# Kernel tuning notes

Measured on AMD Instinct MI355X. Metric: run time of the kernel, lower is better.

## Reference

```python
import jax, jax.numpy as jnp
import numpy as np

N_QUBITS = 12
N_LAYERS = 4
BATCH = 4096
OUT_DIM = 12


def _ry(theta):
    theta = jnp.asarray(theta, jnp.float32)
    c, s = jnp.cos(theta / 2), jnp.sin(theta / 2)
    U = jnp.stack([jnp.stack([c, -s], -1), jnp.stack([s, c], -1)], -2)
    return U.astype(jnp.complex64)


def _rx(theta):
    theta = jnp.asarray(theta, jnp.float32)
    c = jnp.cos(theta / 2).astype(jnp.complex64)
    s = (-1j) * jnp.sin(theta / 2).astype(jnp.complex64)
    return jnp.stack([jnp.stack([c, s], -1), jnp.stack([s, c], -1)], -2)


def _rz(theta):
    theta = jnp.asarray(theta, jnp.float32)
    e = jnp.exp((-0.5j) * theta.astype(jnp.complex64))
    z = jnp.zeros_like(e)
    return jnp.stack([jnp.stack([e, z], -1), jnp.stack([z, jnp.conj(e)], -1)], -2)


def _apply_1q(psi, U, w):
    # psi: (B,) + (2,)*n; U: (2,2) shared gate or (B,2,2) per-sample gate
    psi = jnp.moveaxis(psi, w + 1, 1)
    if U.ndim == 2:
        psi = jnp.einsum('ij,bj...->bi...', U, psi)
    else:
        psi = jnp.einsum('bij,bj...->bi...', U, psi)
    return jnp.moveaxis(psi, 1, w + 1)


def _cnot(psi, c, t):
    # flip target axis where control bit == 1
    psi = jnp.moveaxis(psi, (c + 1, t + 1), (1, 2))
    psi = psi.at[:, 1].set(psi[:, 1, ::-1])
    return jnp.moveaxis(psi, (1, 2), (c + 1, t + 1))


def _pauli_z_signs(n):
    idx = np.arange(2 ** n)
    bits = (idx[None, :] >> (n - 1 - np.arange(n))[:, None]) & 1  # wire 0 = MSB
    return jnp.asarray(1.0 - 2.0 * bits, jnp.float32)  # (n, 2^n)


def _quantum_forward(x, quantum_weights):
    b, n = x.shape[0], N_QUBITS
    # tf.nn.l2_normalize(sample, axis=0) per sample
    xn = x * jax.lax.rsqrt(jnp.maximum(jnp.sum(x * x, axis=1, keepdims=True), 1e-12))
    # angle encoding: pi * x / (max|x| + 1e-8)
    angles = jnp.pi * xn / (jnp.max(jnp.abs(xn), axis=1, keepdims=True) + 1e-8)
    psi = jnp.zeros((b, 2 ** n), jnp.complex64).at[:, 0].set(1.0)
    psi = psi.reshape((b,) + (2,) * n)
    # data encoding: RY(angles[i]) on wire i (per-sample batched gates)
    for i in range(n):
        psi = _apply_1q(psi, _ry(angles[:, i]), i)
    # variational layers: RX/RY/RZ per qubit, then CNOT ring
    for layer in range(N_LAYERS):
        base = layer * 3 * n
        for i in range(n):
            p = base + 3 * i
            psi = _apply_1q(psi, _rx(quantum_weights[p]), i)
            psi = _apply_1q(psi, _ry(quantum_weights[p + 1]), i)
            psi = _apply_1q(psi, _rz(quantum_weights[p + 2]), i)
        for i in range(n):
            psi = _cnot(psi, i, (i + 1) % n)
    psi = psi.reshape(b, -1)
    probs = jnp.real(psi) ** 2 + jnp.imag(psi) ** 2  # (B, 2^n)
    return probs @ _pauli_z_signs(n).T  # (B, n): <Z_i> per qubit


def setup_inputs() -> dict:
    key = jax.random.key(0)
    k1, k2, k3 = jax.random.split(key, 3)
    n_params = 3 * N_QUBITS * N_LAYERS
    return {
        'x': jax.random.normal(k1, (BATCH, N_QUBITS), jnp.float32),
        'quantum_weights': jax.random.uniform(k2, (n_params,), jnp.float32, -0.05, 0.05),
        'dense_w': jax.random.normal(k3, (N_QUBITS, OUT_DIM), jnp.float32) / np.sqrt(N_QUBITS),
        'dense_b': jnp.zeros((OUT_DIM,), jnp.float32),
    }


def reference(x, quantum_weights, dense_w, dense_b):
    q = _quantum_forward(x, quantum_weights)
    return jnp.tanh(q @ dense_w + dense_b)
```

## Files before the change

### kernel.cpp

```cpp
#include <hip/hip_runtime.h>
#include <math.h>

#define NQ   12
#define NL   4
#define GBLK 256
#define QBLK 512
#define SOFF(i) ((i) * 8192)

typedef float v4f  __attribute__((ext_vector_type(4)));
typedef __fp16 v8h __attribute__((ext_vector_type(8)));

__device__ __forceinline__ constexpr int sigma_inv_c(int i) {
    int j = i;
    for (int c = 0; c < NQ; ++c) {
        int t = (c + 1) % NQ;
        int cb = (j >> (NQ - 1 - c)) & 1;
        j ^= cb << (NQ - 1 - t);
    }
    return j;
}

__device__ __forceinline__ constexpr int lswz(int l) {
    return l ^ (((l >> 3) ^ (l >> 7)) & 7);
}

__device__ __forceinline__ unsigned pk2(float a, float b) {
    return __builtin_bit_cast(unsigned, __builtin_amdgcn_cvt_pkrtz(a, b));
}

__device__ __forceinline__ int fslot(int k, int n) {
    return ((k >> 3) * 16 + n) * 8 + (k & 7);
}

__global__ __launch_bounds__(GBLK) void gate_kernel(
    const float* __restrict__ qw, __fp16* __restrict__ gout)
{
    __shared__ float G[NQ][8];
    const int t = threadIdx.x;
    const int mat = blockIdx.x;
    const int layer = mat / 3, ph = mat - 3 * layer;
    if (t < NQ) {
        const int p = layer * 3 * NQ + 3 * t;
        float t1 = qw[p], t2 = qw[p + 1], t3 = qw[p + 2];
        float a, b, c, d, gr, h;
        sincosf(0.5f * t1, &b, &a);
        sincosf(0.5f * t2, &d, &c);
        sincosf(0.5f * t3, &h, &gr);
        float m00r =  c * a, m00i =  d * b;
        float m01r = -d * a, m01i = -c * b;
        float m10r =  d * a, m10i = -c * b;
        float m11r =  c * a, m11i = -d * b;
        float* g = G[t];
        g[0] = gr * m00r + h * m00i;  g[1] = gr * m00i - h * m00r;
        g[2] = gr * m01r + h * m01i;  g[3] = gr * m01i - h * m01r;
        g[4] = gr * m10r - h * m10i;  g[5] = gr * m10i + h * m10r;
        g[6] = gr * m11r - h * m11i;  g[7] = gr * m11i + h * m11r;
    }
    __syncthreads();
    const int n = t & 15, r = t >> 4;
    const int wbase = (ph == 0) ? 8 : (ph == 1) ? 4 : 0;
    float cr = 1.f, ci = 0.f;
    #pragma unroll
    for (int b = 0; b < 4; ++b) {
        const float* g = G[wbase + b];
        const int rb = (r >> (3 - b)) & 1, nb = (n >> (3 - b)) & 1;
        const float er = g[(nb * 2 + rb) * 2], ei = g[(nb * 2 + rb) * 2 + 1];
        const float xr = cr * er - ci * ei, xi = cr * ei + ci * er;
        cr = xr; ci = xi;
    }
    __fp16* b1 = gout + (mat * 2 + 0) * 512;
    __fp16* b2 = gout + (mat * 2 + 1) * 512;
    b1[fslot(2 * r, n)]     = (__fp16)cr;
    b1[fslot(2 * r + 1, n)] = (__fp16)(-ci);
    b2[fslot(2 * r, n)]     = (__fp16)ci;
    b2[fslot(2 * r + 1, n)] = (__fp16)cr;
}

#define READ_FRAGS(AF, SRC)                                                 \
    _Pragma("unroll")                                                       \
    for (int j = 0; j < 2; ++j)                                             \
        AF[j] = __builtin_bit_cast(v8h, *(const uint4*)&sh[(SRC) +          \
                    lswz((((wv) << 6) | ((2 * qh + j) << 4) | nn) * 4 + g) * 8]);

#define BLOAD(MAT)                                                          \
    const v8h b1 = gf[((MAT) * 2 + 0) * 64 + lane];                         \
    const v8h b2 = gf[((MAT) * 2 + 1) * 64 + lane];

#define MFMA_ONE(AF)                                                        \
    _Pragma("unroll")                                                       \
    for (int j = 0; j < 2; ++j) {                                           \
        d1[j] = __builtin_amdgcn_mfma_f32_16x16x32_f16(AF[j], b1, zf, 0, 0, 0); \
        d2[j] = __builtin_amdgcn_mfma_f32_16x16x32_f16(AF[j], b2, zf, 0, 0, 0); \
    }

#define SCHB __builtin_amdgcn_sched_barrier(0);

#define WRITE_COLS(DST)                                                     \
    _Pragma("unroll")                                                       \
    for (int j = 0; j < 2; ++j) {                                           \
        const int CCn = (nn << 4) | (wv << 2) | (2 * qh + j);               \
        *(uint4*)&sh[(DST) + lswz(CCn * 4 + g) * 8] =                       \
            make_uint4(pk2(d1[j].x, d2[j].x), pk2(d1[j].y, d2[j].y),        \
                       pk2(d1[j].z, d2[j].z), pk2(d1[j].w, d2[j].w));       \
    }

#define WRITE_SIGMA(DST)                                                    \
    _Pragma("unroll")                                                       \
    for (int j = 0; j < 2; ++j) {                                           \
        const int iq = ifix ^ (j ? sq1 : sq0);                              \
        _Pragma("unroll")                                                   \
        for (int rg = 0; rg < 4; ++rg) {                                    \
            const int ii = iq ^ sigma_inv_c(rg);                            \
            *(unsigned*)&sh[(DST) + lswz(ii >> 2) * 8 + (ii & 3) * 2] =     \
                pk2(d1[j][rg], d2[j][rg]);                                  \
        }                                                                   \
    }

#define WHT_EPI(OFF)                                                        \
    { float p8[8];                                                          \
      _Pragma("unroll")                                                     \
      for (int j = 0; j < 2; ++j)                                           \
          _Pragma("unroll")                                                 \
          for (int rg = 0; rg < 4; ++rg)                                    \
              p8[j * 4 + rg] = d1[j][rg] * d1[j][rg] + d2[j][rg] * d2[j][rg]; \
      _Pragma("unroll")                                                     \
      for (int st = 1; st < 8; st <<= 1) {                                  \
          _Pragma("unroll")                                                 \
          for (int i = 0; i < 8; ++i) {                                     \
              if (!(i & st)) {                                              \
                  const float a = p8[i], b = p8[i ^ st];                    \
                  p8[i] = a + b; p8[i ^ st] = a - b;                        \
              }                                                             \
          }                                                                 \
      }                                                                     \
      float vals[NQ];                                                       \
      _Pragma("unroll")                                                     \
      for (int w = 0; w < NQ; ++w) {                                        \
          const int sb = 11 - w;                                            \
          const int f3 = (sigma_inv_c(0x20) >> sb) & 1;                     \
          const int f2 = (sigma_inv_c(0x10) >> sb) & 1;                     \
          const int f1 = (sigma_inv_c(2)    >> sb) & 1;                     \
          const int f0 = (sigma_inv_c(1)    >> sb) & 1;                     \
          const float v = p8[f2 * 4 + f1 * 2 + f0];                         \
          const int sgn = ((ifix >> sb) & 1) ^ (f3 & qh);                   \
          vals[w] = sgn ? -v : v;                                           \
      }                                                                     \
      _Pragma("unroll")                                                     \
      for (int m = 1; m <= 8; m <<= 1) {                                    \
          _Pragma("unroll")                                                 \
          for (int w = 0; w < NQ; ++w) vals[w] += __shfl_xor(vals[w], m);   \
      }                                                                     \
      if ((lane & 15) == 0) {                                               \
          _Pragma("unroll")                                                 \
          for (int w = 0; w < NQ; ++w)                                      \
              red[(OFF) + W * 48 + (lane >> 4) * 12 + w] = vals[w];         \
      } }

__global__ __launch_bounds__(QBLK) void qsim_kernel(
    const float* __restrict__ x,
    const __fp16* __restrict__ gates,
    const float* __restrict__ dw,
    const float* __restrict__ db,
    float* __restrict__ out,
    int batch)
{
    __shared__ __align__(16) __fp16 sh[32768];
    float* xv    = (float*)sh;
    float* enc_c = (float*)sh + 64;
    float* enc_s = (float*)sh + 128;
    float* red   = (float*)sh;

    const int tid  = threadIdx.x;
    const int lane = tid & 63;
    const int W    = tid >> 6;
    const int wv   = W & 3;
    const int qh   = W >> 2;
    const int base = 4 * blockIdx.x;
    int ss[4];
    #pragma unroll
    for (int i = 0; i < 4; ++i) {
        int s = base + i;
        ss[i] = (s < batch) ? s : batch - 1;
    }
    const int nn = lane & 15, g = lane >> 4;
    const v8h* gf = (const v8h*)gates;
    const v4f zf = {0.f, 0.f, 0.f, 0.f};

    if (tid < 4 * NQ) {
        const int smp = tid / NQ, j = tid - smp * NQ;
        xv[tid] = x[ss[smp] * NQ + j];
    }
    __syncthreads();
    if (tid < 4 * NQ) {
        const int b0 = (tid / NQ) * NQ;
        float sum = 0.f;
        #pragma unroll
        for (int j = 0; j < NQ; ++j) sum += xv[b0 + j] * xv[b0 + j];
        float inv = rsqrtf(fmaxf(sum, 1e-12f));
        float mx = 0.f;
        #pragma unroll
        for (int j = 0; j < NQ; ++j) mx = fmaxf(mx, fabsf(xv[b0 + j] * inv));
        float ang = 3.14159265358979323846f * (xv[tid] * inv) / (mx + 1e-8f);
        float cc, sn;
        sincosf(0.5f * ang, &sn, &cc);
        enc_c[tid] = cc; enc_s[tid] = sn;
    }
    __syncthreads();

    v8h af0[2], af1[2], af2[2], af3[2];
    #define PICK(SMP, WW, B) ((B) ? enc_s[(SMP) * NQ + (WW)] : enc_c[(SMP) * NQ + (WW)])
    #define INIT_AF(AF, SMP)                                                \
    {   float R4[4];                                                        \
        _Pragma("unroll")                                                   \
        for (int t = 0; t < 4; ++t) {                                       \
            const int r = 4 * g + t;                                        \
            R4[t] = PICK(SMP, 8, (r >> 3) & 1) * PICK(SMP, 9, (r >> 2) & 1) \
                  * PICK(SMP, 10, (r >> 1) & 1) * PICK(SMP, 11, r & 1);     \
        }                                                                   \
        const float Pfix = PICK(SMP, 0, (wv >> 1) & 1) * PICK(SMP, 1, wv & 1) \
                         * PICK(SMP, 4, (nn >> 3) & 1) * PICK(SMP, 5, (nn >> 2) & 1) \
                         * PICK(SMP, 6, (nn >> 1) & 1) * PICK(SMP, 7, nn & 1); \
        _Pragma("unroll")                                                   \
        for (int j = 0; j < 2; ++j) {                                       \
            const float Pq = Pfix * PICK(SMP, 2, qh) * PICK(SMP, 3, j);     \
            _Pragma("unroll")                                               \
            for (int t = 0; t < 4; ++t) {                                   \
                AF[j][2 * t]     = (__fp16)(Pq * R4[t]);                    \
                AF[j][2 * t + 1] = (__fp16)0.f;                             \
            }                                                               \
        }                                                                   \
    }
    INIT_AF(af0, 0)
    INIT_AF(af1, 1)
    INIT_AF(af2, 2)
    INIT_AF(af3, 3)
    #undef PICK
    __syncthreads();

    const int ifix = sigma_inv_c((nn << 8) | (wv << 6) | (g << 2));
    const int sq0 = qh ? sigma_inv_c(0x20) : 0;
    const int sq1 = qh ? sigma_inv_c(0x30) : sigma_inv_c(0x10);

    v4f d1[2], d2[2];
    #define READ4                                                           \
        READ_FRAGS(af0, SOFF(0)) READ_FRAGS(af1, SOFF(1))                   \
        READ_FRAGS(af2, SOFF(2)) READ_FRAGS(af3, SOFF(3))
    #define COLS4(MAT)                                                      \
        { BLOAD(MAT)                                                        \
          MFMA_ONE(af0) WRITE_COLS(SOFF(0)) SCHB                            \
          MFMA_ONE(af1) WRITE_COLS(SOFF(1)) SCHB                            \
          MFMA_ONE(af2) WRITE_COLS(SOFF(2)) SCHB                            \
          MFMA_ONE(af3) WRITE_COLS(SOFF(3)) }
    #define SIGMA4(MAT)                                                     \
        { BLOAD(MAT)                                                        \
          MFMA_ONE(af0) WRITE_SIGMA(SOFF(0)) SCHB                           \
          MFMA_ONE(af1) WRITE_SIGMA(SOFF(1)) SCHB                           \
          MFMA_ONE(af2) WRITE_SIGMA(SOFF(2)) SCHB                           \
          MFMA_ONE(af3) WRITE_SIGMA(SOFF(3)) }

    #pragma unroll 1
    for (int l = 0; l < NL; ++l) {
        if (l > 0) {
            READ4
            __syncthreads();
        }
        COLS4(l * 3 + 0)
        __syncthreads();

        READ4
        __syncthreads();
        COLS4(l * 3 + 1)
        __syncthreads();

        READ4
        __syncthreads();
        if (l < NL - 1) {
            SIGMA4(l * 3 + 2)
            __syncthreads();
        } else {
            { BLOAD(l * 3 + 2)
              MFMA_ONE(af0) WHT_EPI(0)    SCHB
              MFMA_ONE(af1) WHT_EPI(384)  SCHB
              MFMA_ONE(af2) WHT_EPI(768)  SCHB
              MFMA_ONE(af3) WHT_EPI(1152) }
        }
    }

    __syncthreads();
    if (tid < 4 * NQ) {
        const int smp = tid / NQ, w = tid - smp * NQ;
        float acc = 0.f;
        #pragma unroll
        for (int k = 0; k < 32; ++k) acc += red[smp * 384 + k * 12 + w];
        red[1536 + tid] = acc;
    }
    __syncthreads();
    if (tid < 4 * NQ) {
        const int smp = tid / NQ, o = tid - smp * NQ;
        const float* rv = red + 1536 + smp * NQ;
        float v = db[o];
        #pragma unroll
        for (int w = 0; w < NQ; ++w) v += rv[w] * dw[w * NQ + o];
        out[ss[smp] * NQ + o] = tanhf(v);
    }
}

extern "C" void kernel_launch(void* const* d_in, const int* in_sizes, int n_in,
                              void* d_out, int out_size, void* d_ws, size_t ws_size,
                              hipStream_t stream) {
    const float* x  = (const float*)d_in[0];
    const float* qw = (const float*)d_in[1];
    const float* dw = (const float*)d_in[2];
    const float* db = (const float*)d_in[3];
    float* out = (float*)d_out;
    __fp16* gates = (__fp16*)d_ws;
    int batch = in_sizes[0] / NQ;
    int nblk = (batch + 3) / 4;
    gate_kernel<<<12, GBLK, 0, stream>>>(qw, gates);
    qsim_kernel<<<nblk, QBLK, 0, stream>>>(x, gates, dw, db, out, batch);
}
```

Baseline: 115.5 us.

## Chain second and third gate-group MFMAs in registers, skipping an LDS round-trip

The second and third 4-qubit gate matrices of each layer are now applied back to back. The first MFMA's accumulator output is packed directly into A-operand fragments for the next MFMA, which works because the MFMA output layout matches the input fragment layout for this index mapping. This removes one LDS write, one LDS read of the full state and two block barriers per layer. In exchange, the sigma-permutation write and the Walsh-Hadamard epilogue index mappings had to be re-derived, and correctness depends on that new mapping.

```diff
diff --git a/kernel.cpp b/kernel.cpp
--- a/kernel.cpp
+++ b/kernel.cpp
@@ -9,6 +9,7 @@
 
 typedef float v4f  __attribute__((ext_vector_type(4)));
 typedef __fp16 v8h __attribute__((ext_vector_type(8)));
+typedef unsigned v4u __attribute__((ext_vector_type(4)));
 
 __device__ __forceinline__ constexpr int sigma_inv_c(int i) {
     int j = i;
@@ -86,11 +87,33 @@
     const v8h b1 = gf[((MAT) * 2 + 0) * 64 + lane];                         \
     const v8h b2 = gf[((MAT) * 2 + 1) * 64 + lane];
 
+#define BLOAD2(MATB, MATC)                                                  \
+    const v8h b1 = gf[((MATB) * 2 + 0) * 64 + lane];                        \
+    const v8h b2 = gf[((MATB) * 2 + 1) * 64 + lane];                        \
+    const v8h c1 = gf[((MATC) * 2 + 0) * 64 + lane];                        \
+    const v8h c2 = gf[((MATC) * 2 + 1) * 64 + lane];
+
 #define MFMA_ONE(AF)                                                        \
     _Pragma("unroll")                                                       \
     for (int j = 0; j < 2; ++j) {                                           \
         d1[j] = __builtin_amdgcn_mfma_f32_16x16x32_f16(AF[j], b1, zf, 0, 0, 0); \
         d2[j] = __builtin_amdgcn_mfma_f32_16x16x32_f16(AF[j], b2, zf, 0, 0, 0); \
+    }
+
+#define PACK_AF(AF)                                                         \
+    _Pragma("unroll")                                                       \
+    for (int j = 0; j < 2; ++j) {                                           \
+        v4u t;                                                              \
+        _Pragma("unroll")                                                   \
+        for (int rg = 0; rg < 4; ++rg) t[rg] = pk2(d1[j][rg], d2[j][rg]);   \
+        AF[j] = __builtin_bit_cast(v8h, t);                                 \
+    }
+
+#define MFMA_CC(AF)                                                         \
+    _Pragma("unroll")                                                       \
+    for (int j = 0; j < 2; ++j) {                                           \
+        d1[j] = __builtin_amdgcn_mfma_f32_16x16x32_f16(AF[j], c1, zf, 0, 0, 0); \
+        d2[j] = __builtin_amdgcn_mfma_f32_16x16x32_f16(AF[j], c2, zf, 0, 0, 0); \
     }
 
 #define SCHB __builtin_amdgcn_sched_barrier(0);
@@ -104,19 +127,19 @@
                        pk2(d1[j].z, d2[j].z), pk2(d1[j].w, d2[j].w));       \
     }
 
-#define WRITE_SIGMA(DST)                                                    \
-    _Pragma("unroll")                                                       \
-    for (int j = 0; j < 2; ++j) {                                           \
-        const int iq = ifix ^ (j ? sq1 : sq0);                              \
+#define WRITE_SIGMA2(DST)                                                   \
+    _Pragma("unroll")                                                       \
+    for (int j = 0; j < 2; ++j) {                                           \
+        const int ij = ifix2 ^ (j ? sigma_inv_c(1) : 0);                    \
         _Pragma("unroll")                                                   \
         for (int rg = 0; rg < 4; ++rg) {                                    \
-            const int ii = iq ^ sigma_inv_c(rg);                            \
+            const int ii = ij ^ sigma_inv_c(rg << 4);                       \
             *(unsigned*)&sh[(DST) + lswz(ii >> 2) * 8 + (ii & 3) * 2] =     \
                 pk2(d1[j][rg], d2[j][rg]);                                  \
         }                                                                   \
     }
 
-#define WHT_EPI(OFF)                                                        \
+#define WHT_EPI2(OFF)                                                       \
     { float p8[8];                                                          \
       _Pragma("unroll")                                                     \
       for (int j = 0; j < 2; ++j)                                           \
@@ -137,13 +160,11 @@
       _Pragma("unroll")                                                     \
       for (int w = 0; w < NQ; ++w) {                                        \
           const int sb = 11 - w;                                            \
-          const int f3 = (sigma_inv_c(0x20) >> sb) & 1;                     \
-          const int f2 = (sigma_inv_c(0x10) >> sb) & 1;                     \
-          const int f1 = (sigma_inv_c(2)    >> sb) & 1;                     \
-          const int f0 = (sigma_inv_c(1)    >> sb) & 1;                     \
-          const float v = p8[f2 * 4 + f1 * 2 + f0];                         \
-          const int sgn = ((ifix >> sb) & 1) ^ (f3 & qh);                   \
-          vals[w] = sgn ? -v : v;                                           \
+          const int fj  = (sigma_inv_c(0x001) >> sb) & 1;                   \
+          const int frh = (sigma_inv_c(0x020) >> sb) & 1;                   \
+          const int frl = (sigma_inv_c(0x010) >> sb) & 1;                   \
+          const float v = p8[fj * 4 + frh * 2 + frl];                       \
+          vals[w] = ((ifix2 >> sb) & 1) ? -v : v;                           \
       }                                                                     \
       _Pragma("unroll")                                                     \
       for (int m = 1; m <= 8; m <<= 1) {                                    \
@@ -237,9 +258,7 @@
     #undef PICK
     __syncthreads();
 
-    const int ifix = sigma_inv_c((nn << 8) | (wv << 6) | (g << 2));
-    const int sq0 = qh ? sigma_inv_c(0x20) : 0;
-    const int sq1 = qh ? sigma_inv_c(0x30) : sigma_inv_c(0x10);
+    const int ifix2 = sigma_inv_c((nn << 8) | (g << 6) | (wv << 2) | (qh << 1));
 
     v4f d1[2], d2[2];
     #define READ4                                                           \
@@ -251,12 +270,10 @@
           MFMA_ONE(af1) WRITE_COLS(SOFF(1)) SCHB                            \
           MFMA_ONE(af2) WRITE_COLS(SOFF(2)) SCHB                            \
           MFMA_ONE(af3) WRITE_COLS(SOFF(3)) }
-    #define SIGMA4(MAT)                                                     \
-        { BLOAD(MAT)                                                        \
-          MFMA_ONE(af0) WRITE_SIGMA(SOFF(0)) SCHB                           \
-          MFMA_ONE(af1) WRITE_SIGMA(SOFF(1)) SCHB                           \
-          MFMA_ONE(af2) WRITE_SIGMA(SOFF(2)) SCHB                           \
-          MFMA_ONE(af3) WRITE_SIGMA(SOFF(3)) }
+    #define CHAIN_S(AF, DST)                                                \
+        MFMA_ONE(AF) PACK_AF(AF) MFMA_CC(AF) WRITE_SIGMA2(DST)
+    #define CHAIN_E(AF, EOFF)                                               \
+        MFMA_ONE(AF) PACK_AF(AF) MFMA_CC(AF) WHT_EPI2(EOFF)
 
     #pragma unroll 1
     for (int l = 0; l < NL; ++l) {
@@ -269,20 +286,19 @@
 
         READ4
         __syncthreads();
-        COLS4(l * 3 + 1)
-        __syncthreads();
-
-        READ4
-        __syncthreads();
         if (l < NL - 1) {
-            SIGMA4(l * 3 + 2)
+            { BLOAD2(l * 3 + 1, l * 3 + 2)
+              CHAIN_S(af0, SOFF(0)) SCHB
+              CHAIN_S(af1, SOFF(1)) SCHB
+              CHAIN_S(af2, SOFF(2)) SCHB
+              CHAIN_S(af3, SOFF(3)) }
             __syncthreads();
         } else {
-            { BLOAD(l * 3 + 2)
-              MFMA_ONE(af0) WHT_EPI(0)    SCHB
-              MFMA_ONE(af1) WHT_EPI(384)  SCHB
-              MFMA_ONE(af2) WHT_EPI(768)  SCHB
-              MFMA_ONE(af3) WHT_EPI(1152) }
+            { BLOAD2(l * 3 + 1, l * 3 + 2)
+              CHAIN_E(af0, 0)    SCHB
+              CHAIN_E(af1, 384)  SCHB
+              CHAIN_E(af2, 768)  SCHB
+              CHAIN_E(af3, 1152) }
         }
     }
 
```

Result: faster. 107.9 us (-6.6%).
